# Performance work log

Hardware: AMD Instinct MI355X
Metric: run time of the kernel (lower is better)

Reference implementation:

```python
import jax, jax.numpy as jnp
import numpy as np
from jax import lax

B, Cin, C, H, W, Ns, K = 2, 64, 64, 256, 1216, 20000, 9
HW = H * W
D = 2 * C + 3   # 131, MLP input dim
Dh = D // 2     # 65, MLP hidden dim


def _conv(x, w, b, relu):
    y = lax.conv_general_dilated(x, w, (1, 1), 'SAME',
                                 dimension_numbers=('NCHW', 'OIHW', 'NCHW'))
    y = y + b[None, :, None, None]
    return jax.nn.relu(y) if relu else y


def _mlp(f, w1, b1, w2, b2):
    # f: (B, Ns, K, D) -> (B, Ns, K, 1)
    h = jax.nn.leaky_relu(f @ w1 + b1, 0.2)
    return h @ w2 + b2


def setup_inputs() -> dict:
    ks = jax.random.split(jax.random.key(0), 32)
    s = 0.05
    rng = np.random.default_rng(0)
    # unique point indices per batch (torch scatter with dup indices is nondeterministic)
    pc = np.stack([np.sort(rng.choice(HW, Ns, replace=False)) for _ in range(B)])[:, None, :]
    inp = {
        'rgb': jax.random.normal(ks[0], (B, Cin, H, W), jnp.float32),
        'sdepth': jax.random.normal(ks[1], (B, Cin, H, W), jnp.float32),
        'pc_idx': jnp.asarray(pc, dtype=jnp.int32),
        'nbrs_idx': jax.random.randint(ks[2], (B, 1, Ns, K), 0, HW, dtype=jnp.int32),
        'nbrs_disp': jax.random.normal(ks[3], (B, 3, Ns, K), jnp.float32),
        'd_conv0_w': jax.random.normal(ks[4], (C, Cin, 3, 3), jnp.float32) * s,
        'd_conv0_b': jnp.zeros((C,), jnp.float32),
        'd_conv1_w': jax.random.normal(ks[5], (C, Cin, 3, 3), jnp.float32) * s,
        'd_conv1_b': jnp.zeros((C,), jnp.float32),
        'd_conv2_w': jax.random.normal(ks[6], (C, C, 3, 3), jnp.float32) * s,
        'd_conv2_b': jnp.zeros((C,), jnp.float32),
        'r_conv0_w': jax.random.normal(ks[7], (C, Cin, 3, 3), jnp.float32) * s,
        'r_conv0_b': jnp.zeros((C,), jnp.float32),
        'r_conv1_w': jax.random.normal(ks[8], (C, Cin, 3, 3), jnp.float32) * s,
        'r_conv1_b': jnp.zeros((C,), jnp.float32),
        'r_conv2_w': jax.random.normal(ks[9], (C, C, 3, 3), jnp.float32) * s,
        'r_conv2_b': jnp.zeros((C,), jnp.float32),
        'd_w1': jax.random.normal(ks[10], (D, Dh), jnp.float32) * s,
        'd_b1': jnp.zeros((Dh,), jnp.float32),
        'd_w2': jax.random.normal(ks[11], (Dh, 1), jnp.float32) * s,
        'd_b2': jnp.zeros((1,), jnp.float32),
        'r_w1': jax.random.normal(ks[12], (D, Dh), jnp.float32) * s,
        'r_b1': jnp.zeros((Dh,), jnp.float32),
        'r_w2': jax.random.normal(ks[13], (Dh, 1), jnp.float32) * s,
        'r_b2': jnp.zeros((1,), jnp.float32),
        'd_bias': jnp.zeros((C,), jnp.float32),
        'r_bias': jnp.zeros((C,), jnp.float32),
    }
    return inp


def reference(rgb, sdepth, pc_idx, nbrs_idx, nbrs_disp,
              d_conv0_w, d_conv0_b, d_conv1_w, d_conv1_b, d_conv2_w, d_conv2_b,
              r_conv0_w, r_conv0_b, r_conv1_w, r_conv1_b, r_conv2_w, r_conv2_b,
              d_w1, d_b1, d_w2, d_b2, r_w1, r_b1, r_w2, r_b2, d_bias, r_bias):
    d0 = _conv(sdepth, d_conv0_w, d_conv0_b, True)
    d1 = _conv(sdepth, d_conv1_w, d_conv1_b, False)
    r0 = _conv(rgb, r_conv0_w, r_conv0_b, True)
    r1 = _conv(rgb, r_conv1_w, r_conv1_b, False)

    d0f = d0.reshape(B, C, HW)
    r0f = r0.reshape(B, C, HW)

    pcb = jnp.broadcast_to(pc_idx, (B, C, Ns))
    nb = jnp.broadcast_to(nbrs_idx.reshape(B, 1, Ns * K), (B, C, Ns * K))
    d_s = jnp.take_along_axis(d0f, pcb, axis=2)                       # (B,C,Ns)
    d_nn = jnp.take_along_axis(d0f, nb, axis=2).reshape(B, C, Ns, K)  # (B,C,Ns,K)
    r_s = jnp.take_along_axis(r0f, pcb, axis=2)
    # NOTE: faithful to source, r neighbors are gathered from d_feat0
    r_nn = jnp.take_along_axis(d0f, nb, axis=2).reshape(B, C, Ns, K)

    feats = jnp.concatenate([d_nn - d_s[..., None],
                             r_nn - r_s[..., None],
                             nbrs_disp], axis=1)                      # (B,2C+3,Ns,K)
    feats = jnp.moveaxis(feats, 1, -1)                                # (B,Ns,K,2C+3)

    d_attn = jax.nn.softmax(_mlp(feats, d_w1, d_b1, d_w2, d_b2)[..., 0], axis=-1)  # (B,Ns,K)
    r_attn = jax.nn.softmax(_mlp(feats, r_w1, r_b1, r_w2, r_b2)[..., 0], axis=-1)

    d_feat = jnp.einsum('bnk,bcnk->bcn', d_attn, d_nn) + d_bias[None, :, None]
    r_feat = jnp.einsum('bnk,bcnk->bcn', r_attn, r_nn) + r_bias[None, :, None]

    scat = jax.vmap(lambda idx, src: jnp.zeros((C, HW), src.dtype).at[:, idx].set(src))
    d_new = scat(pc_idx[:, 0], d_feat)
    r_new = scat(pc_idx[:, 0], r_feat)

    # mask scatter in source uses index of shape (B,1,Ns): only channel 0 is set
    mask0 = jax.vmap(lambda i: jnp.zeros((HW,), d0f.dtype).at[i].set(1.0))(pc_idx[:, 0])
    masks = jnp.concatenate([mask0[:, None, :], jnp.zeros((B, C - 1, HW), d0f.dtype)], axis=1)

    d0f = (1.0 - masks) * d0f + d_new
    r0f = (1.0 - masks) * r0f + r_new

    d2 = _conv(d0f.reshape(B, C, H, W), d_conv2_w, d_conv2_b, False)
    r2 = _conv(r0f.reshape(B, C, H, W), r_conv2_w, r_conv2_b, False)
    return jax.nn.relu(d2 + d1), jax.nn.relu(r2 + r1)
```

## Files before the change

### kernel.cpp

```cpp
#include <hip/hip_runtime.h>

#define H_ 256
#define W_ 1216
#define HW_ (H_*W_)
#define B_ 2
#define Ns_ 20000
#define K_ 9
#define D_ 131
#define Dh_ 65

#define TPOS 66

typedef __attribute__((ext_vector_type(8))) short bf16x8;
typedef __attribute__((ext_vector_type(4))) float f32x4;

__device__ __forceinline__ float b2f(unsigned short u){
  union { unsigned int i; float f; } v; v.i = ((unsigned int)u) << 16; return v.f;
}
__device__ __forceinline__ unsigned short f2b(float f){
  union { float f; unsigned int i; } v; v.f = f;
  unsigned int r = (v.i + 0x7FFFu + ((v.i >> 16) & 1u)) >> 16;
  return (unsigned short)r;
}

struct WPtrs { const float* w[6]; };

__global__ void prep_w(WPtrs wp, unsigned short* __restrict__ Asw){
  int blk = blockIdx.x;
  int c = blk / 72, rem = blk % 72, mt = rem / 18, kc = rem % 18;
  int lane = threadIdx.x;
  const float* w = wp.w[c];
  int co = mt*16 + (lane & 15);
  int kb = kc*32 + (lane >> 4)*8;
  unsigned short* dst = Asw + ((size_t)blk*64 + lane)*8;
  #pragma unroll
  for (int j = 0; j < 8; ++j){
    int k = kb + j, tap = k >> 6, cin = k & 63;
    dst[j] = f2b(w[((size_t)co*64 + cin)*9 + tap]);
  }
}

__global__ void prep_wmlp(const float* __restrict__ dw1, const float* __restrict__ rw1,
                          unsigned short* __restrict__ Bm){
  int blk = blockIdx.x;
  int nt = blk / 5, ks = blk % 5;
  int lane = threadIdx.x;
  int col = nt*16 + (lane & 15);
  int kb  = ks*32 + (lane >> 4)*8;
  unsigned short* dst = Bm + ((size_t)blk*64 + lane)*8;
  #pragma unroll
  for (int jj = 0; jj < 8; ++jj){
    int row = kb + jj;
    float v = 0.f;
    if (row < D_ && col < 2*Dh_)
      v = (col < Dh_) ? dw1[(size_t)row*Dh_ + col] : rw1[(size_t)row*Dh_ + (col - Dh_)];
    dst[jj] = f2b(v);
  }
}

__global__ __launch_bounds__(256) void transpose_in(
    const float* __restrict__ x, unsigned short* __restrict__ xt)
{
  __shared__ unsigned short t[128*64];
  int tid = threadIdx.x, l = tid & 63, w = tid >> 6;
  int b = blockIdx.y;
  size_t p0 = (size_t)blockIdx.x * 128;
  int pos = (w & 1)*64 + l;
  const float* src = x + (size_t)b*64*HW_ + p0 + pos;
  #pragma unroll
  for (int it = 0; it < 4; ++it){
    int c8 = (w >> 1)*4 + it;
    union { unsigned short us[8]; uint4 v; } pk;
    #pragma unroll
    for (int j = 0; j < 8; ++j)
      pk.us[j] = f2b(src[(size_t)(c8*8 + j)*HW_]);
    *(uint4*)&t[pos*64 + ((c8 ^ (pos & 7)) << 3)] = pk.v;
  }
  __syncthreads();
  unsigned short* dst = xt + ((size_t)b*HW_ + p0)*64;
  #pragma unroll
  for (int it = 0; it < 4; ++it){
    int e = it*256 + tid;
    int pp = e >> 3, sl = e & 7;
    *(uint4*)&dst[(size_t)pp*64 + sl*8] =
        *(const uint4*)&t[pp*64 + ((sl ^ (pp & 7)) << 3)];
  }
}

__global__ __launch_bounds__(256,4) void conv01_mfma(
    const unsigned short* __restrict__ xt,
    const unsigned short* __restrict__ Asw,
    const float* __restrict__ b0, const float* __restrict__ b1,
    unsigned short* __restrict__ y0t, unsigned short* __restrict__ u,
    float* __restrict__ y1out)
{
  __shared__ unsigned short tile[4*TPOS*64];
  int tid = threadIdx.x;
  int c0 = blockIdx.x*64, r0 = blockIdx.y*2, b = blockIdx.z;

  for (int e = tid; e < 4*TPOS*8; e += 256){
    int pos = e >> 3, ch = e & 7;
    int row = pos / TPOS, col = pos - row*TPOS;
    int gy = r0 - 1 + row, gx = c0 - 1 + col;
    uint4 v = {0u,0u,0u,0u};
    if (gy >= 0 && gy < H_ && gx >= 0 && gx < W_)
      v = *(const uint4*)&xt[((size_t)b*HW_ + (size_t)gy*W_ + gx)*64 + ch*8];
    *(uint4*)&tile[pos*64 + ((ch ^ (pos & 7)) << 3)] = v;
  }
  __syncthreads();

  int wave = tid >> 6, lane = tid & 63;
  int quad = lane >> 4, l15 = lane & 15;
  int cobase = (wave & 1)*32;
  int prow = wave >> 1;

  f32x4 acc[2][2][4];
  #pragma unroll
  for (int cv = 0; cv < 2; ++cv)
    #pragma unroll
    for (int mt = 0; mt < 2; ++mt)
      #pragma unroll
      for (int nt = 0; nt < 4; ++nt)
        acc[cv][mt][nt] = (f32x4){0.f,0.f,0.f,0.f};

  const unsigned short* Ap[2][2];
  #pragma unroll
  for (int cv = 0; cv < 2; ++cv)
    #pragma unroll
    for (int mt = 0; mt < 2; ++mt)
      Ap[cv][mt] = Asw + ((size_t)((cv*4 + (wave&1)*2 + mt)*18)*64 + lane)*8;

  #pragma unroll
  for (int tap = 0; tap < 9; ++tap){
    int pbase = (prow + tap/3)*TPOS + l15 + (tap%3);
    int pk = pbase & 7;
    #pragma unroll
    for (int cc = 0; cc < 2; ++cc){
      int kc = tap*2 + cc;
      int sl = ((quad + 4*cc) ^ pk) << 3;
      bf16x8 a[2][2], bb[4];
      #pragma unroll
      for (int cv = 0; cv < 2; ++cv)
        #pragma unroll
        for (int mt = 0; mt < 2; ++mt)
          a[cv][mt] = *(const bf16x8*)(Ap[cv][mt] + (size_t)kc*512);
      #pragma unroll
      for (int nt = 0; nt < 4; ++nt)
        bb[nt] = *(const bf16x8*)&tile[(pbase + nt*16)*64 + sl];
      #pragma unroll
      for (int cv = 0; cv < 2; ++cv)
        #pragma unroll
        for (int mt = 0; mt < 2; ++mt)
          #pragma unroll
          for (int nt = 0; nt < 4; ++nt)
            acc[cv][mt][nt] = __builtin_amdgcn_mfma_f32_16x16x32_bf16(
                a[cv][mt], bb[nt], acc[cv][mt][nt], 0, 0, 0);
    }
  }

  int gy = r0 + prow;
  #pragma unroll
  for (int mt = 0; mt < 2; ++mt){
    int co4 = cobase + mt*16 + quad*4;
    f32x4 bias0 = *(const f32x4*)&b0[co4];
    f32x4 bias1 = *(const f32x4*)&b1[co4];
    #pragma unroll
    for (int nt = 0; nt < 4; ++nt){
      int gx = c0 + nt*16 + l15;
      size_t gpix = (size_t)gy*W_ + gx;
      f32x4 v0 = acc[0][mt][nt] + bias0;
      ushort4 q;
      q.x = f2b(fmaxf(v0.x,0.f)); q.y = f2b(fmaxf(v0.y,0.f));
      q.z = f2b(fmaxf(v0.z,0.f)); q.w = f2b(fmaxf(v0.w,0.f));
      size_t toff = ((size_t)b*HW_ + gpix)*64 + co4;
      *(ushort4*)&y0t[toff] = q;
      *(ushort4*)&u[toff]   = q;
      f32x4 v1 = acc[1][mt][nt] + bias1;
      float* yo = y1out + ((size_t)b*64 + co4)*HW_ + gpix;
      yo[(size_t)0*HW_] = v1.x; yo[(size_t)1*HW_] = v1.y;
      yo[(size_t)2*HW_] = v1.z; yo[(size_t)3*HW_] = v1.w;
    }
  }
}

__global__ __launch_bounds__(256,4) void conv2_mfma(
    const unsigned short* __restrict__ ut,
    const unsigned short* __restrict__ Asw,
    const float* __restrict__ bias,
    float* __restrict__ out)
{
  __shared__ unsigned short tile[4*TPOS*64];
  int tid = threadIdx.x;
  int c0 = blockIdx.x*64, r0 = blockIdx.y*2, b = blockIdx.z;

  for (int e = tid; e < 4*TPOS*8; e += 256){
    int pos = e >> 3, ch = e & 7;
    int row = pos / TPOS, col = pos - row*TPOS;
    int gy = r0 - 1 + row, gx = c0 - 1 + col;
    uint4 v = {0u,0u,0u,0u};
    if (gy >= 0 && gy < H_ && gx >= 0 && gx < W_)
      v = *(const uint4*)&ut[((size_t)b*HW_ + (size_t)gy*W_ + gx)*64 + ch*8];
    *(uint4*)&tile[pos*64 + ((ch ^ (pos & 7)) << 3)] = v;
  }
  __syncthreads();

  int wave = tid >> 6, lane = tid & 63;
  int quad = lane >> 4, l15 = lane & 15;
  int cobase = (wave & 1)*32;
  int prow = wave >> 1;

  f32x4 acc[2][4];
  #pragma unroll
  for (int mt = 0; mt < 2; ++mt)
    #pragma unroll
    for (int nt = 0; nt < 4; ++nt)
      acc[mt][nt] = (f32x4){0.f,0.f,0.f,0.f};

  const unsigned short* Ap[2];
  #pragma unroll
  for (int mt = 0; mt < 2; ++mt)
    Ap[mt] = Asw + ((size_t)(((wave&1)*2 + mt)*18)*64 + lane)*8;

  #pragma unroll
  for (int tap = 0; tap < 9; ++tap){
    int pbase = (prow + tap/3)*TPOS + l15 + (tap%3);
    int pk = pbase & 7;
    #pragma unroll
    for (int cc = 0; cc < 2; ++cc){
      int kc = tap*2 + cc;
      int sl = ((quad + 4*cc) ^ pk) << 3;
      bf16x8 a[2], bb[4];
      #pragma unroll
      for (int mt = 0; mt < 2; ++mt)
        a[mt] = *(const bf16x8*)(Ap[mt] + (size_t)kc*512);
      #pragma unroll
      for (int nt = 0; nt < 4; ++nt)
        bb[nt] = *(const bf16x8*)&tile[(pbase + nt*16)*64 + sl];
      #pragma unroll
      for (int mt = 0; mt < 2; ++mt)
        #pragma unroll
        for (int nt = 0; nt < 4; ++nt)
          acc[mt][nt] = __builtin_amdgcn_mfma_f32_16x16x32_bf16(
              a[mt], bb[nt], acc[mt][nt], 0, 0, 0);
    }
  }

  int gy = r0 + prow;
  #pragma unroll
  for (int mt = 0; mt < 2; ++mt){
    int co4 = cobase + mt*16 + quad*4;
    f32x4 bs = *(const f32x4*)&bias[co4];
    #pragma unroll
    for (int nt = 0; nt < 4; ++nt){
      int gx = c0 + nt*16 + l15;
      size_t gpix = (size_t)gy*W_ + gx;
      float* yo = out + ((size_t)b*64 + co4)*HW_ + gpix;
      f32x4 v = acc[mt][nt] + bs;
      float r0v = v.x + yo[(size_t)0*HW_];
      float r1v = v.y + yo[(size_t)1*HW_];
      float r2v = v.z + yo[(size_t)2*HW_];
      float r3v = v.w + yo[(size_t)3*HW_];
      yo[(size_t)0*HW_] = r0v > 0.f ? r0v : 0.f;
      yo[(size_t)1*HW_] = r1v > 0.f ? r1v : 0.f;
      yo[(size_t)2*HW_] = r2v > 0.f ? r2v : 0.f;
      yo[(size_t)3*HW_] = r3v > 0.f ? r3v : 0.f;
    }
  }
}

#define FBSTR 176
#define AW 4

struct __align__(16) WaveShm {
  unsigned short featsB[16][FBSTR];
  float feats[9][64];
  float ds[64], rs[64];
  float attnw[2][12];
};

__global__ __launch_bounds__(256) void attn_kernel(
    const unsigned short* __restrict__ d0t, const unsigned short* __restrict__ r0t,
    const int* __restrict__ pc_idx, const int* __restrict__ nbrs_idx,
    const float* __restrict__ disp,
    const unsigned short* __restrict__ Bmlp,
    const float* __restrict__ db2v, const float* __restrict__ dw2,
    const float* __restrict__ rb2v, const float* __restrict__ rw2,
    const float* __restrict__ dbias, const float* __restrict__ rbias,
    unsigned short* __restrict__ u_d, unsigned short* __restrict__ u_r)
{
  __shared__ WaveShm shm[AW];
  int tid = threadIdx.x;
  int wave = tid >> 6, lane = tid & 63;
  int quad = lane >> 4, l15 = lane & 15;
  int n = blockIdx.x * AW + wave;
  int b = blockIdx.y;
  WaveShm& S = shm[wave];

  int s = pc_idx[(size_t)b*Ns_ + n];
  s = __builtin_amdgcn_readfirstlane(s);

  int myidx = (lane < 9) ? nbrs_idx[((size_t)b*Ns_ + n)*K_ + lane] : 0;
  int idx8 = __shfl(myidx, 8);

  {
    uint4 z = {0u,0u,0u,0u};
    unsigned short* fb = &S.featsB[0][0];
    #pragma unroll
    for (int it = 0; it < 6; ++it){
      int e = it*64 + lane;
      if (e < 16*FBSTR/8) *(uint4*)&fb[e*8] = z;
    }
  }
  if (lane < 27){
    int m = lane / 9, k = lane - m*9;
    S.featsB[k][128 + m] = f2b(disp[(((size_t)b*3 + m)*Ns_ + n)*K_ + k]);
  }

  int grow = lane >> 3, gp = lane & 7;
  int gidx = __shfl(myidx, grow);
  uint4 g1 = *(const uint4*)&d0t[((size_t)b*HW_ + (size_t)gidx)*64 + gp*8];
  uint4 g2 = {0u,0u,0u,0u};
  if (lane < 24){
    int r2 = 8 + grow;
    int idx2 = (r2 == 8) ? idx8 : s;
    const unsigned short* base = (r2 == 10) ? r0t : d0t;
    g2 = *(const uint4*)&base[((size_t)b*HW_ + (size_t)idx2)*64 + gp*8];
  }

  float dn[8];
  {
    const unsigned short* us = (const unsigned short*)&g1;
    #pragma unroll
    for (int j = 0; j < 8; ++j){ dn[j] = b2f(us[j]); S.feats[grow][gp*8 + j] = dn[j]; }
  }
  if (lane >= 8 && lane < 24){
    const unsigned short* us = (const unsigned short*)&g2;
    float* dst = (lane < 16) ? &S.ds[(lane - 8)*8] : &S.rs[(lane - 16)*8];
    #pragma unroll
    for (int j = 0; j < 8; ++j) dst[j] = b2f(us[j]);
  }

  {
    unsigned short od[8], orr[8];
    #pragma unroll
    for (int j = 0; j < 8; ++j){
      int c = gp*8 + j;
      od[j]  = f2b(dn[j] - S.ds[c]);
      orr[j] = f2b(dn[j] - S.rs[c]);
    }
    *(uint4*)&S.featsB[grow][gp*8]      = *(uint4*)od;
    *(uint4*)&S.featsB[grow][64 + gp*8] = *(uint4*)orr;
  }
  if (lane < 8){
    const unsigned short* us = (const unsigned short*)&g2;
    unsigned short od[8], orr[8];
    #pragma unroll
    for (int j = 0; j < 8; ++j){
      int c = lane*8 + j;
      float v = b2f(us[j]);
      S.feats[8][c] = v;
      od[j]  = f2b(v - S.ds[c]);
      orr[j] = f2b(v - S.rs[c]);
    }
    *(uint4*)&S.featsB[8][lane*8]      = *(uint4*)od;
    *(uint4*)&S.featsB[8][64 + lane*8] = *(uint4*)orr;
  }

  bf16x8 afr[5];
  #pragma unroll
  for (int ks = 0; ks < 5; ++ks)
    afr[ks] = *(const bf16x8*)&S.featsB[l15][ks*32 + quad*8];

  float pd[2][4];
  #pragma unroll
  for (int m = 0; m < 2; ++m)
    #pragma unroll
    for (int r = 0; r < 4; ++r) pd[m][r] = 0.f;

  #pragma unroll
  for (int nt = 0; nt < 9; ++nt){
    f32x4 acc = (f32x4){0.f,0.f,0.f,0.f};
    const unsigned short* bp = Bmlp + ((size_t)nt*5*64 + lane)*8;
    #pragma unroll
    for (int ks = 0; ks < 5; ++ks){
      bf16x8 bfr = *(const bf16x8*)(bp + (size_t)ks*512);
      acc = __builtin_amdgcn_mfma_f32_16x16x32_bf16(afr[ks], bfr, acc, 0, 0, 0);
    }
    int jq = nt*16 + l15;
    if (jq < 2*Dh_){
      int mlp = (jq >= Dh_) ? 1 : 0;
      int j = jq - mlp*Dh_;
      float w2 = mlp ? rw2[j] : dw2[j];
      #pragma unroll
      for (int r = 0; r < 4; ++r){
        float h = acc[r];
        h = h > 0.f ? h : 0.2f*h;
        pd[mlp][r] += h * w2;
      }
    }
  }

  #pragma unroll
  for (int mask = 1; mask <= 8; mask <<= 1)
    #pragma unroll
    for (int m = 0; m < 2; ++m)
      #pragma unroll
      for (int r = 0; r < 4; ++r)
        pd[m][r] += __shfl_xor(pd[m][r], mask);

  float b2c[2] = { db2v[0], rb2v[0] };
  #pragma unroll
  for (int m = 0; m < 2; ++m){
    float lg[4];
    float mx = -3.4e38f;
    #pragma unroll
    for (int r = 0; r < 4; ++r){
      lg[r] = pd[m][r] + b2c[m];
      if (quad*4 + r < 9) mx = fmaxf(mx, lg[r]);
    }
    mx = fmaxf(mx, __shfl_xor(mx, 16));
    mx = fmaxf(mx, __shfl_xor(mx, 32));
    float ex[4], sum = 0.f;
    #pragma unroll
    for (int r = 0; r < 4; ++r){
      int k = quad*4 + r;
      ex[r] = (k < 9) ? __expf(lg[r] - mx) : 0.f;
      sum += ex[r];
    }
    sum += __shfl_xor(sum, 16);
    sum += __shfl_xor(sum, 32);
    float inv = 1.f / sum;
    if (l15 == 0){
      #pragma unroll
      for (int r = 0; r < 4; ++r){
        int k = quad*4 + r;
        if (k < 9) S.attnw[m][k] = ex[r] * inv;
      }
    }
  }

  {
    int c = lane;
    #pragma unroll
    for (int m = 0; m < 2; ++m){
      float f = (m ? rbias : dbias)[c];
      #pragma unroll
      for (int k = 0; k < 9; ++k)
        f += S.attnw[m][k] * S.feats[k][c];
      float base = (c == 0) ? 0.f : (m ? S.rs[c] : S.ds[c]);
      unsigned short* u = m ? u_r : u_d;
      u[((size_t)b*HW_ + (size_t)s)*64 + c] = f2b(base + f);
    }
  }
}

extern "C" void kernel_launch(void* const* d_in, const int* in_sizes, int n_in,
                              void* d_out, int out_size, void* d_ws, size_t ws_size,
                              hipStream_t stream)
{
  (void)in_sizes; (void)n_in; (void)out_size; (void)ws_size;

  const float* rgb       = (const float*)d_in[0];
  const float* sdepth    = (const float*)d_in[1];
  const int*   pc_idx    = (const int*)d_in[2];
  const int*   nbrs_idx  = (const int*)d_in[3];
  const float* nbrs_disp = (const float*)d_in[4];

  WPtrs wp;
  wp.w[0] = (const float*)d_in[5];
  wp.w[1] = (const float*)d_in[7];
  wp.w[2] = (const float*)d_in[9];
  wp.w[3] = (const float*)d_in[11];
  wp.w[4] = (const float*)d_in[13];
  wp.w[5] = (const float*)d_in[15];
  const float* d_conv0_b = (const float*)d_in[6];
  const float* d_conv1_b = (const float*)d_in[8];
  const float* d_conv2_b = (const float*)d_in[10];
  const float* r_conv0_b = (const float*)d_in[12];
  const float* r_conv1_b = (const float*)d_in[14];
  const float* r_conv2_b = (const float*)d_in[16];
  const float* d_w1 = (const float*)d_in[17];
  const float* d_w2 = (const float*)d_in[19];
  const float* d_b2 = (const float*)d_in[20];
  const float* r_w1 = (const float*)d_in[21];
  const float* r_w2 = (const float*)d_in[23];
  const float* r_b2 = (const float*)d_in[24];
  const float* d_bias = (const float*)d_in[25];
  const float* r_bias = (const float*)d_in[26];

  char* ws = (char*)d_ws;
  const size_t TSZ = (size_t)B_ * HW_ * 64 * 2;
  unsigned short* u_d = (unsigned short*)(ws + 0*TSZ);
  unsigned short* u_r = (unsigned short*)(ws + 1*TSZ);
  unsigned short* d0t = (unsigned short*)(ws + 2*TSZ);
  unsigned short* r0t = (unsigned short*)(ws + 3*TSZ);
  unsigned short* xt  = (unsigned short*)(ws + 4*TSZ);
  unsigned short* Asw = (unsigned short*)(ws + 5*TSZ);
  const size_t CONV_STRIDE = 4*18*64*8;
  unsigned short* Bmlp = Asw + 6*CONV_STRIDE;

  prep_w<<<432, 64, 0, stream>>>(wp, Asw);
  prep_wmlp<<<45, 64, 0, stream>>>(d_w1, r_w1, Bmlp);

  float* out = (float*)d_out;
  const size_t OUTSZ = (size_t)B_ * 64 * HW_;

  dim3 cgrid(W_/64, H_/2, B_);
  dim3 tgrid(HW_/128, B_);

  transpose_in<<<tgrid, 256, 0, stream>>>(sdepth, xt);
  conv01_mfma<<<cgrid, 256, 0, stream>>>(xt, Asw + 0*CONV_STRIDE,
      d_conv0_b, d_conv1_b, d0t, u_d, out);
  transpose_in<<<tgrid, 256, 0, stream>>>(rgb, xt);
  conv01_mfma<<<cgrid, 256, 0, stream>>>(xt, Asw + 3*CONV_STRIDE,
      r_conv0_b, r_conv1_b, r0t, u_r, out + OUTSZ);

  attn_kernel<<<dim3(Ns_/AW, B_), 256, 0, stream>>>(
      d0t, r0t, pc_idx, nbrs_idx, nbrs_disp,
      Bmlp,
      d_b2, d_w2, r_b2, r_w2,
      d_bias, r_bias,
      u_d, u_r);

  conv2_mfma<<<cgrid, 256, 0, stream>>>(u_d, Asw + 2*CONV_STRIDE, d_conv2_b, out);
  conv2_mfma<<<cgrid, 256, 0, stream>>>(u_r, Asw + 5*CONV_STRIDE, r_conv2_b, out + OUTSZ);
}
```

Measured before the change: 1.364 ms.

## Fuse input transpose into conv01, store conv1 residual as fp16, merge launches

Drops the separate transpose_in kernels: conv01 now reads NCHW fp32 input directly, converts it to bf16 and writes the swizzled LDS tile itself. The conv1 output is stored as channels-last fp16 instead of fp32 NCHW in the output buffer, and conv2 reads it from there for the residual add. The depth and rgb branches share one grid per conv stage (z=4), and conv2 fills its tile with direct global-to-LDS loads. The aim is to cut HBM traffic and launch count. In exchange, the input reads in conv01 are strided and re-fetched in halo regions, and the fp16 residual adds rounding error.

```diff
diff --git a/kernel.cpp b/kernel.cpp
--- a/kernel.cpp
+++ b/kernel.cpp
@@ -10,6 +10,7 @@
 #define Dh_ 65
 
 #define TPOS 66
+#define CSTR (4*18*64*8)
 
 typedef __attribute__((ext_vector_type(8))) short bf16x8;
 typedef __attribute__((ext_vector_type(4))) float f32x4;
@@ -21,6 +22,17 @@
   union { float f; unsigned int i; } v; v.f = f;
   unsigned int r = (v.i + 0x7FFFu + ((v.i >> 16) & 1u)) >> 16;
   return (unsigned short)r;
+}
+__device__ __forceinline__ unsigned short f2h(float f){
+  union { _Float16 h; unsigned short u; } v; v.h = (_Float16)f; return v.u;
+}
+__device__ __forceinline__ float h2f(unsigned short u){
+  union { _Float16 h; unsigned short u; } v; v.u = u; return (float)v.h;
+}
+__device__ __forceinline__ void gld_lds16(const void* g, void* l){
+  __builtin_amdgcn_global_load_lds(
+      (const __attribute__((address_space(1))) unsigned int*)g,
+      (__attribute__((address_space(3))) unsigned int*)l, 16, 0, 0);
 }
 
 struct WPtrs { const float* w[6]; };
@@ -58,54 +70,37 @@
   }
 }
 
-__global__ __launch_bounds__(256) void transpose_in(
-    const float* __restrict__ x, unsigned short* __restrict__ xt)
-{
-  __shared__ unsigned short t[128*64];
-  int tid = threadIdx.x, l = tid & 63, w = tid >> 6;
-  int b = blockIdx.y;
-  size_t p0 = (size_t)blockIdx.x * 128;
-  int pos = (w & 1)*64 + l;
-  const float* src = x + (size_t)b*64*HW_ + p0 + pos;
-  #pragma unroll
-  for (int it = 0; it < 4; ++it){
-    int c8 = (w >> 1)*4 + it;
-    union { unsigned short us[8]; uint4 v; } pk;
-    #pragma unroll
-    for (int j = 0; j < 8; ++j)
-      pk.us[j] = f2b(src[(size_t)(c8*8 + j)*HW_]);
-    *(uint4*)&t[pos*64 + ((c8 ^ (pos & 7)) << 3)] = pk.v;
-  }
-  __syncthreads();
-  unsigned short* dst = xt + ((size_t)b*HW_ + p0)*64;
-  #pragma unroll
-  for (int it = 0; it < 4; ++it){
-    int e = it*256 + tid;
-    int pp = e >> 3, sl = e & 7;
-    *(uint4*)&dst[(size_t)pp*64 + sl*8] =
-        *(const uint4*)&t[pp*64 + ((sl ^ (pp & 7)) << 3)];
-  }
-}
-
 __global__ __launch_bounds__(256,4) void conv01_mfma(
-    const unsigned short* __restrict__ xt,
+    const float* __restrict__ xd, const float* __restrict__ xr,
     const unsigned short* __restrict__ Asw,
-    const float* __restrict__ b0, const float* __restrict__ b1,
-    unsigned short* __restrict__ y0t, unsigned short* __restrict__ u,
-    float* __restrict__ y1out)
+    const float* __restrict__ b0d, const float* __restrict__ b1d,
+    const float* __restrict__ b0r, const float* __restrict__ b1r,
+    unsigned short* __restrict__ d0t, unsigned short* __restrict__ u_d,
+    unsigned short* __restrict__ r0t, unsigned short* __restrict__ u_r,
+    unsigned short* __restrict__ y1h_d, unsigned short* __restrict__ y1h_r)
 {
   __shared__ unsigned short tile[4*TPOS*64];
   int tid = threadIdx.x;
-  int c0 = blockIdx.x*64, r0 = blockIdx.y*2, b = blockIdx.z;
+  int c0 = blockIdx.x*64, r0 = blockIdx.y*2;
+  int t = blockIdx.z >> 1, b = blockIdx.z & 1;
+
+  const float* x = t ? xr : xd;
+  const unsigned short* Aswt = Asw + (size_t)(t ? 3 : 0)*CSTR;
 
   for (int e = tid; e < 4*TPOS*8; e += 256){
-    int pos = e >> 3, ch = e & 7;
+    int pos = e >> 3, slot = e & 7;
     int row = pos / TPOS, col = pos - row*TPOS;
     int gy = r0 - 1 + row, gx = c0 - 1 + col;
-    uint4 v = {0u,0u,0u,0u};
-    if (gy >= 0 && gy < H_ && gx >= 0 && gx < W_)
-      v = *(const uint4*)&xt[((size_t)b*HW_ + (size_t)gy*W_ + gx)*64 + ch*8];
-    *(uint4*)&tile[pos*64 + ((ch ^ (pos & 7)) << 3)] = v;
+    int c8 = slot ^ (pos & 7);
+    union { unsigned short us[8]; uint4 v; } pk;
+    if (gy >= 0 && gy < H_ && gx >= 0 && gx < W_){
+      const float* sp = x + ((size_t)b*64 + c8*8)*HW_ + (size_t)gy*W_ + gx;
+      #pragma unroll
+      for (int j = 0; j < 8; ++j) pk.us[j] = f2b(sp[(size_t)j*HW_]);
+    } else {
+      pk.v = (uint4){0u,0u,0u,0u};
+    }
+    *(uint4*)&tile[pos*64 + slot*8] = pk.v;
   }
   __syncthreads();
 
@@ -128,7 +123,7 @@
   for (int cv = 0; cv < 2; ++cv)
     #pragma unroll
     for (int mt = 0; mt < 2; ++mt)
-      Ap[cv][mt] = Asw + ((size_t)((cv*4 + (wave&1)*2 + mt)*18)*64 + lane)*8;
+      Ap[cv][mt] = Aswt + ((size_t)((cv*4 + (wave&1)*2 + mt)*18)*64 + lane)*8;
 
   #pragma unroll
   for (int tap = 0; tap < 9; ++tap){
@@ -158,6 +153,12 @@
     }
   }
 
+  unsigned short* y0t = t ? r0t : d0t;
+  unsigned short* u   = t ? u_r  : u_d;
+  unsigned short* y1h = t ? y1h_r : y1h_d;
+  const float* b0 = t ? b0r : b0d;
+  const float* b1 = t ? b1r : b1d;
+
   int gy = r0 + prow;
   #pragma unroll
   for (int mt = 0; mt < 2; ++mt){
@@ -168,39 +169,58 @@
     for (int nt = 0; nt < 4; ++nt){
       int gx = c0 + nt*16 + l15;
       size_t gpix = (size_t)gy*W_ + gx;
+      size_t toff = ((size_t)b*HW_ + gpix)*64 + co4;
       f32x4 v0 = acc[0][mt][nt] + bias0;
       ushort4 q;
       q.x = f2b(fmaxf(v0.x,0.f)); q.y = f2b(fmaxf(v0.y,0.f));
       q.z = f2b(fmaxf(v0.z,0.f)); q.w = f2b(fmaxf(v0.w,0.f));
-      size_t toff = ((size_t)b*HW_ + gpix)*64 + co4;
       *(ushort4*)&y0t[toff] = q;
       *(ushort4*)&u[toff]   = q;
       f32x4 v1 = acc[1][mt][nt] + bias1;
-      float* yo = y1out + ((size_t)b*64 + co4)*HW_ + gpix;
-      yo[(size_t)0*HW_] = v1.x; yo[(size_t)1*HW_] = v1.y;
-      yo[(size_t)2*HW_] = v1.z; yo[(size_t)3*HW_] = v1.w;
+      ushort4 h;
+      h.x = f2h(v1.x); h.y = f2h(v1.y); h.z = f2h(v1.z); h.w = f2h(v1.w);
+      *(ushort4*)&y1h[toff] = h;
     }
   }
 }
 
 __global__ __launch_bounds__(256,4) void conv2_mfma(
-    const unsigned short* __restrict__ ut,
+    const unsigned short* __restrict__ u_d, const unsigned short* __restrict__ u_r,
     const unsigned short* __restrict__ Asw,
-    const float* __restrict__ bias,
+    const float* __restrict__ biasd, const float* __restrict__ biasr,
+    const unsigned short* __restrict__ y1h_d, const unsigned short* __restrict__ y1h_r,
     float* __restrict__ out)
 {
   __shared__ unsigned short tile[4*TPOS*64];
   int tid = threadIdx.x;
-  int c0 = blockIdx.x*64, r0 = blockIdx.y*2, b = blockIdx.z;
-
-  for (int e = tid; e < 4*TPOS*8; e += 256){
-    int pos = e >> 3, ch = e & 7;
-    int row = pos / TPOS, col = pos - row*TPOS;
-    int gy = r0 - 1 + row, gx = c0 - 1 + col;
-    uint4 v = {0u,0u,0u,0u};
-    if (gy >= 0 && gy < H_ && gx >= 0 && gx < W_)
-      v = *(const uint4*)&ut[((size_t)b*HW_ + (size_t)gy*W_ + gx)*64 + ch*8];
-    *(uint4*)&tile[pos*64 + ((ch ^ (pos & 7)) << 3)] = v;
+  int c0 = blockIdx.x*64, r0 = blockIdx.y*2;
+  int t = blockIdx.z >> 1, b = blockIdx.z & 1;
+
+  const unsigned short* ut  = t ? u_r : u_d;
+  const unsigned short* y1h = t ? y1h_r : y1h_d;
+  const unsigned short* Aswt = Asw + (size_t)(t ? 5 : 2)*CSTR;
+  const float* bias = t ? biasr : biasd;
+  float* o = out + (size_t)t * B_ * 64 * HW_;
+
+  {
+    int wave = tid >> 6, lane = tid & 63;
+    #pragma unroll 1
+    for (int it = 0; it < 9; ++it){
+      int e = wave*528 + it*64 + lane;
+      bool active = (it < 8) || (lane < 16);
+      if (active){
+        int pos = e >> 3, slot = e & 7;
+        int row = pos / TPOS, col = pos - row*TPOS;
+        int gy = r0 - 1 + row, gx = c0 - 1 + col;
+        int c8 = slot ^ (pos & 7);
+        if (gy >= 0 && gy < H_ && gx >= 0 && gx < W_){
+          const unsigned short* src = &ut[((size_t)b*HW_ + (size_t)gy*W_ + gx)*64 + c8*8];
+          gld_lds16(src, &tile[(size_t)(wave*528 + it*64)*8]);
+        } else {
+          *(uint4*)&tile[(size_t)e*8] = (uint4){0u,0u,0u,0u};
+        }
+      }
+    }
   }
   __syncthreads();
 
@@ -219,7 +239,7 @@
   const unsigned short* Ap[2];
   #pragma unroll
   for (int mt = 0; mt < 2; ++mt)
-    Ap[mt] = Asw + ((size_t)(((wave&1)*2 + mt)*18)*64 + lane)*8;
+    Ap[mt] = Aswt + ((size_t)(((wave&1)*2 + mt)*18)*64 + lane)*8;
 
   #pragma unroll
   for (int tap = 0; tap < 9; ++tap){
@@ -254,12 +274,13 @@
     for (int nt = 0; nt < 4; ++nt){
       int gx = c0 + nt*16 + l15;
       size_t gpix = (size_t)gy*W_ + gx;
-      float* yo = out + ((size_t)b*64 + co4)*HW_ + gpix;
+      ushort4 h = *(const ushort4*)&y1h[((size_t)b*HW_ + gpix)*64 + co4];
       f32x4 v = acc[mt][nt] + bs;
-      float r0v = v.x + yo[(size_t)0*HW_];
-      float r1v = v.y + yo[(size_t)1*HW_];
-      float r2v = v.z + yo[(size_t)2*HW_];
-      float r3v = v.w + yo[(size_t)3*HW_];
+      float r0v = v.x + h2f(h.x);
+      float r1v = v.y + h2f(h.y);
+      float r2v = v.z + h2f(h.z);
+      float r3v = v.w + h2f(h.w);
+      float* yo = o + ((size_t)b*64 + co4)*HW_ + gpix;
       yo[(size_t)0*HW_] = r0v > 0.f ? r0v : 0.f;
       yo[(size_t)1*HW_] = r1v > 0.f ? r1v : 0.f;
       yo[(size_t)2*HW_] = r2v > 0.f ? r2v : 0.f;
@@ -490,30 +511,25 @@
 
   char* ws = (char*)d_ws;
   const size_t TSZ = (size_t)B_ * HW_ * 64 * 2;
-  unsigned short* u_d = (unsigned short*)(ws + 0*TSZ);
-  unsigned short* u_r = (unsigned short*)(ws + 1*TSZ);
-  unsigned short* d0t = (unsigned short*)(ws + 2*TSZ);
-  unsigned short* r0t = (unsigned short*)(ws + 3*TSZ);
-  unsigned short* xt  = (unsigned short*)(ws + 4*TSZ);
-  unsigned short* Asw = (unsigned short*)(ws + 5*TSZ);
-  const size_t CONV_STRIDE = 4*18*64*8;
-  unsigned short* Bmlp = Asw + 6*CONV_STRIDE;
+  unsigned short* u_d   = (unsigned short*)(ws + 0*TSZ);
+  unsigned short* u_r   = (unsigned short*)(ws + 1*TSZ);
+  unsigned short* d0t   = (unsigned short*)(ws + 2*TSZ);
+  unsigned short* r0t   = (unsigned short*)(ws + 3*TSZ);
+  unsigned short* y1h_d = (unsigned short*)(ws + 4*TSZ);
+  unsigned short* y1h_r = (unsigned short*)(ws + 5*TSZ);
+  unsigned short* Asw   = (unsigned short*)(ws + 6*TSZ);
+  unsigned short* Bmlp  = Asw + 6*CSTR;
 
   prep_w<<<432, 64, 0, stream>>>(wp, Asw);
   prep_wmlp<<<45, 64, 0, stream>>>(d_w1, r_w1, Bmlp);
 
   float* out = (float*)d_out;
-  const size_t OUTSZ = (size_t)B_ * 64 * HW_;
-
-  dim3 cgrid(W_/64, H_/2, B_);
-  dim3 tgrid(HW_/128, B_);
-
-  transpose_in<<<tgrid, 256, 0, stream>>>(sdepth, xt);
-  conv01_mfma<<<cgrid, 256, 0, stream>>>(xt, Asw + 0*CONV_STRIDE,
-      d_conv0_b, d_conv1_b, d0t, u_d, out);
-  transpose_in<<<tgrid, 256, 0, stream>>>(rgb, xt);
-  conv01_mfma<<<cgrid, 256, 0, stream>>>(xt, Asw + 3*CONV_STRIDE,
-      r_conv0_b, r_conv1_b, r0t, u_r, out + OUTSZ);
+
+  dim3 cgrid(W_/64, H_/2, 4);
+
+  conv01_mfma<<<cgrid, 256, 0, stream>>>(sdepth, rgb, Asw,
+      d_conv0_b, d_conv1_b, r_conv0_b, r_conv1_b,
+      d0t, u_d, r0t, u_r, y1h_d, y1h_r);
 
   attn_kernel<<<dim3(Ns_/AW, B_), 256, 0, stream>>>(
       d0t, r0t, pc_idx, nbrs_idx, nbrs_disp,
@@ -522,6 +538,6 @@
       d_bias, r_bias,
       u_d, u_r);
 
-  conv2_mfma<<<cgrid, 256, 0, stream>>>(u_d, Asw + 2*CONV_STRIDE, d_conv2_b, out);
-  conv2_mfma<<<cgrid, 256, 0, stream>>>(u_r, Asw + 5*CONV_STRIDE, r_conv2_b, out + OUTSZ);
-}
+  conv2_mfma<<<cgrid, 256, 0, stream>>>(u_d, u_r, Asw,
+      d_conv2_b, r_conv2_b, y1h_d, y1h_r, out);
+}
```

Result: faster. 1.260 ms (-7.6%).
